# Performance work log

Measured on AMD Instinct MI355X. Metric: run time of the kernel, lower is better.

## Reference

```python
import jax, jax.numpy as jnp
import numpy as np

BETA = 5.5
MEM_FILLED = 25  # number of occupied slots per class; remaining slots are zero (empty)


def setup_inputs() -> dict:
    key = jax.random.key(0)
    ks = jax.random.split(key, 7)
    C, M, D = 1000, 50, 1024
    mem = jax.random.normal(ks[0], (C, M, D), jnp.float32)
    # emulate a partially-filled memory bank: slots >= MEM_FILLED are empty (all-zero rows)
    mem = mem * (jnp.arange(M)[None, :, None] < MEM_FILLED)
    return {
        "img_feat": jax.random.normal(ks[1], (1, D), jnp.float32),
        "image_feature_memory": mem,
        "fixed_global_feat_vanilla": jax.random.normal(ks[2], (C, 1, D), jnp.float32),
        "global_bias": 0.01 * jax.random.normal(ks[3], (C, D), jnp.float32),
        "global_bias_key": 0.01 * jax.random.normal(ks[4], (C, D), jnp.float32),
        "global_bias_value": 0.01 * jax.random.normal(ks[5], (C, D), jnp.float32),
        "global_ffn_bias": 0.01 * jax.random.normal(ks[6], (C, D), jnp.float32),
        "logit_scale": jnp.asarray(np.log(100.0), dtype=jnp.float32),
    }


def _l2norm(x, axis=-1):
    return x / jnp.linalg.norm(x, axis=axis, keepdims=True)


def reference(img_feat, image_feature_memory, fixed_global_feat_vanilla,
              global_bias, global_bias_key, global_bias_value,
              global_ffn_bias, logit_scale):
    # DualMem.get_image_pred, args.position == 'all', similarity_weighted classifier
    sg = jax.lax.stop_gradient  # torch.no_grad() block
    mem = jnp.concatenate([image_feature_memory, fixed_global_feat_vanilla], axis=1)  # (C, M+1, D)

    q = img_feat + jnp.mean(global_bias, axis=0, keepdims=True)      # (1, D)
    K = mem + global_bias_key[:, None, :]                             # (C, M+1, D)
    V = mem + global_bias_value[:, None, :]                           # (C, M+1, D)

    empty = (jnp.sum(mem, axis=-1) == 0)[..., None]                   # (C, M+1, 1) empty slots
    Kn = jnp.where(empty, 0.0, _l2norm(K))
    Vn = jnp.where(empty, 0.0, _l2norm(V))
    qn = _l2norm(q)
    qn, Kn, Vn = sg(qn), sg(Kn), sg(Vn)

    sim = jnp.exp(-BETA * (1.0 - jnp.einsum('d,cmd->cm', qn[0], Kn)))  # (C, M+1)
    adaptive = jnp.einsum('cm,cmd->cd', sim, Vn)                       # (C, D)
    adaptive = _l2norm(adaptive)
    adaptive = adaptive[None] + global_ffn_bias[None]                  # (1, C, D) position in {'output','all'}
    adaptive = _l2norm(adaptive)

    logits = jnp.exp(logit_scale) * jnp.einsum('bcd,bd->bc', adaptive, img_feat)  # (1, C)
    return jax.nn.softmax(logits, axis=1)
```

## Files before the change

### kernel.cpp

```cpp
#include <hip/hip_runtime.h>
#include <math.h>

#define BETA 5.5f
#define NC 1000
#define NM 51
#define ND 1024

typedef float nt_float4 __attribute__((ext_vector_type(4)));

__device__ __forceinline__ float wave_reduce_sum(float v) {
#pragma unroll
    for (int off = 32; off >= 1; off >>= 1) v += __shfl_xor(v, off, 64);
    return v;
}

__device__ __forceinline__ float block_reduce_sum(float v, float* red, int w, int lane) {
    v = wave_reduce_sum(v);
    __syncthreads();
    if (lane == 0) red[w] = v;
    __syncthreads();
    return red[0] + red[1] + red[2] + red[3];
}

__global__ __launch_bounds__(256) void colsum_part(const float* __restrict__ gb,
                                                   float* __restrict__ qpart) {
    const int t = threadIdx.x;
    const float4* p = (const float4*)(gb + (size_t)blockIdx.x * 25 * ND) + t;
    float4 s = make_float4(0.f, 0.f, 0.f, 0.f);
#pragma unroll
    for (int c = 0; c < 25; ++c) {
        float4 v = p[c * (ND / 4)];
        s.x += v.x; s.y += v.y; s.z += v.z; s.w += v.w;
    }
    ((float4*)qpart)[blockIdx.x * (ND / 4) + t] = s;
}

__global__ __launch_bounds__(256) void qnorm_kernel(const float* __restrict__ img,
                                                    const float* __restrict__ qpart,
                                                    float* __restrict__ qn) {
    __shared__ float red[8];
    const int t = threadIdx.x, w = t >> 6, lane = t & 63;
    float4 s = make_float4(0.f, 0.f, 0.f, 0.f);
#pragma unroll
    for (int p = 0; p < 40; ++p) {
        float4 v = ((const float4*)qpart)[p * (ND / 4) + t];
        s.x += v.x; s.y += v.y; s.z += v.z; s.w += v.w;
    }
    float4 iv = ((const float4*)img)[t];
    float4 q;
    q.x = iv.x + s.x * (1.f / NC);
    q.y = iv.y + s.y * (1.f / NC);
    q.z = iv.z + s.z * (1.f / NC);
    q.w = iv.w + s.w * (1.f / NC);
    float ssq = block_reduce_sum(q.x * q.x + q.y * q.y + q.z * q.z + q.w * q.w, red, w, lane);
    float r = rsqrtf(ssq);
    float4 o = make_float4(q.x * r, q.y * r, q.z * r, q.w * r);
    ((float4*)qn)[t] = o;
}

__global__ __launch_bounds__(256) void dualmem_main(
    const float* __restrict__ mem,
    const float* __restrict__ fixedg,
    const float* __restrict__ qn_g,
    const float* __restrict__ gbk,
    const float* __restrict__ gbv,
    float* __restrict__ accpart)
{
    __shared__ float lds_acc[4 * ND];

    const int c = blockIdx.x >> 1;
    const int half = blockIdx.x & 1;
    const int t = threadIdx.x;
    const int w = t >> 6;
    const int lane = t & 63;
    const int ww = half * 4 + w;

    float4 qn[4], bk[4], bv[4], acc[4];
    const float* bkp = gbk + (size_t)c * ND;
    const float* bvp = gbv + (size_t)c * ND;
#pragma unroll
    for (int j = 0; j < 4; ++j) {
        qn[j] = ((const float4*)qn_g)[j * 64 + lane];
        bk[j] = ((const float4*)bkp)[j * 64 + lane];
        bv[j] = ((const float4*)bvp)[j * 64 + lane];
        acc[j] = make_float4(0.f, 0.f, 0.f, 0.f);
    }

    nt_float4 cur[4], nxt[4];
    {
        const nt_float4* r = (ww < 50) ? (const nt_float4*)(mem + ((size_t)c * 50 + ww) * ND)
                                       : (const nt_float4*)(fixedg + (size_t)c * ND);
#pragma unroll
        for (int j = 0; j < 4; ++j) cur[j] = __builtin_nontemporal_load(&r[j * 64 + lane]);
    }

    for (int m = ww; m < NM; m += 8) {
        const int mn = m + 8;
        if (mn < NM) {
            const nt_float4* r = (mn < 50) ? (const nt_float4*)(mem + ((size_t)c * 50 + mn) * ND)
                                           : (const nt_float4*)(fixedg + (size_t)c * ND);
#pragma unroll
            for (int j = 0; j < 4; ++j) nxt[j] = __builtin_nontemporal_load(&r[j * 64 + lane]);
        }

        float sm = 0.f, ssqK = 0.f, dotK = 0.f, ssqV = 0.f;
#pragma unroll
        for (int j = 0; j < 4; ++j) {
            nt_float4 v = cur[j];
            sm += v.x + v.y + v.z + v.w;
            float kx = v.x + bk[j].x, ky = v.y + bk[j].y, kz = v.z + bk[j].z, kw = v.w + bk[j].w;
            ssqK += kx * kx + ky * ky + kz * kz + kw * kw;
            dotK += qn[j].x * kx + qn[j].y * ky + qn[j].z * kz + qn[j].w * kw;
            float vx = v.x + bv[j].x, vy = v.y + bv[j].y, vz = v.z + bv[j].z, vw = v.w + bv[j].w;
            ssqV += vx * vx + vy * vy + vz * vz + vw * vw;
        }
        sm   = wave_reduce_sum(sm);
        ssqK = wave_reduce_sum(ssqK);
        dotK = wave_reduce_sum(dotK);
        ssqV = wave_reduce_sum(ssqV);
        if (sm != 0.f) {
            float simv = expf(-BETA * (1.f - dotK * rsqrtf(ssqK)));
            float wt = simv * rsqrtf(ssqV);
#pragma unroll
            for (int j = 0; j < 4; ++j) {
                acc[j].x += wt * (cur[j].x + bv[j].x);
                acc[j].y += wt * (cur[j].y + bv[j].y);
                acc[j].z += wt * (cur[j].z + bv[j].z);
                acc[j].w += wt * (cur[j].w + bv[j].w);
            }
        }
#pragma unroll
        for (int j = 0; j < 4; ++j) cur[j] = nxt[j];
    }

#pragma unroll
    for (int j = 0; j < 4; ++j)
        ((float4*)lds_acc)[w * 256 + j * 64 + lane] = acc[j];
    __syncthreads();

    float4 a = make_float4(0.f, 0.f, 0.f, 0.f);
#pragma unroll
    for (int wv = 0; wv < 4; ++wv) {
        float4 p = ((float4*)lds_acc)[wv * 256 + t];
        a.x += p.x; a.y += p.y; a.z += p.z; a.w += p.w;
    }
    ((float4*)(accpart + (size_t)blockIdx.x * ND))[t] = a;
}

__global__ __launch_bounds__(256) void finalize_kernel(
    const float* __restrict__ img,
    const float* __restrict__ accpart,
    const float* __restrict__ ffn,
    const float* __restrict__ lsp,
    float* __restrict__ logits)
{
    __shared__ float red[8];
    const int c = blockIdx.x;
    const int t = threadIdx.x;
    const int w = t >> 6;
    const int lane = t & 63;

    float4 a0 = ((const float4*)(accpart + (size_t)(2 * c) * ND))[t];
    float4 a1 = ((const float4*)(accpart + (size_t)(2 * c + 1) * ND))[t];
    float4 a;
    a.x = a0.x + a1.x; a.y = a0.y + a1.y; a.z = a0.z + a1.z; a.w = a0.w + a1.w;

    float ssqA = block_reduce_sum(a.x * a.x + a.y * a.y + a.z * a.z + a.w * a.w, red, w, lane);
    float arn = rsqrtf(ssqA);
    float4 fv = ((const float4*)(ffn + (size_t)c * ND))[t];
    a.x = a.x * arn + fv.x;
    a.y = a.y * arn + fv.y;
    a.z = a.z * arn + fv.z;
    a.w = a.w * arn + fv.w;
    float ssqB = block_reduce_sum(a.x * a.x + a.y * a.y + a.z * a.z + a.w * a.w, red, w, lane);
    float brn = rsqrtf(ssqB);

    float4 iv = ((const float4*)img)[t];
    float dp = a.x * iv.x + a.y * iv.y + a.z * iv.z + a.w * iv.w;
    dp = block_reduce_sum(dp, red, w, lane);

    if (t == 0) logits[c] = expf(lsp[0]) * dp * brn;
}

__global__ __launch_bounds__(256) void softmax_kernel(const float* __restrict__ logits,
                                                      float* __restrict__ out) {
    __shared__ float red[8];
    int t = threadIdx.x, w = t >> 6, lane = t & 63;
    float l[4];
#pragma unroll
    for (int i = 0; i < 4; ++i) {
        int idx = t * 4 + i;
        l[i] = (idx < NC) ? logits[idx] : -3.402823466e+38f;
    }
    float mx = fmaxf(fmaxf(l[0], l[1]), fmaxf(l[2], l[3]));
#pragma unroll
    for (int off = 32; off >= 1; off >>= 1) mx = fmaxf(mx, __shfl_xor(mx, off, 64));
    __syncthreads();
    if (lane == 0) red[w] = mx;
    __syncthreads();
    mx = fmaxf(fmaxf(red[0], red[1]), fmaxf(red[2], red[3]));
    __syncthreads();

    float e[4], s = 0.f;
#pragma unroll
    for (int i = 0; i < 4; ++i) {
        int idx = t * 4 + i;
        e[i] = (idx < NC) ? expf(l[i] - mx) : 0.f;
        s += e[i];
    }
    s = block_reduce_sum(s, red, w, lane);
    float inv = 1.f / s;
#pragma unroll
    for (int i = 0; i < 4; ++i) {
        int idx = t * 4 + i;
        if (idx < NC) out[idx] = e[i] * inv;
    }
}

extern "C" void kernel_launch(void* const* d_in, const int* in_sizes, int n_in,
                              void* d_out, int out_size, void* d_ws, size_t ws_size,
                              hipStream_t stream) {
    const float* img    = (const float*)d_in[0];
    const float* mem    = (const float*)d_in[1];
    const float* fixedg = (const float*)d_in[2];
    const float* gb     = (const float*)d_in[3];
    const float* gbk    = (const float*)d_in[4];
    const float* gbv    = (const float*)d_in[5];
    const float* ffn    = (const float*)d_in[6];
    const float* ls     = (const float*)d_in[7];

    float* ws      = (float*)d_ws;
    float* qpart   = ws;
    float* qn      = ws + 40 * ND;
    float* accpart = ws + 41 * ND;
    float* logits  = accpart + 2000 * ND;
    float* out     = (float*)d_out;

    colsum_part<<<40, 256, 0, stream>>>(gb, qpart);
    qnorm_kernel<<<1, 256, 0, stream>>>(img, qpart, qn);
    dualmem_main<<<2 * NC, 256, 0, stream>>>(mem, fixedg, qn, gbk, gbv, accpart);
    finalize_kernel<<<NC, 256, 0, stream>>>(img, accpart, ffn, ls, logits);
    softmax_kernel<<<1, 256, 0, stream>>>(logits, out);
}
```

Baseline: 303.1 us.

## Fuse per-class memory attention with finalize into one 512-thread block

```diff
diff --git a/kernel.cpp b/kernel.cpp
--- a/kernel.cpp
+++ b/kernel.cpp
@@ -14,12 +14,20 @@
     return v;
 }
 
-__device__ __forceinline__ float block_reduce_sum(float v, float* red, int w, int lane) {
+__device__ __forceinline__ float block_reduce_sum4(float v, float* red, int w, int lane) {
     v = wave_reduce_sum(v);
     __syncthreads();
     if (lane == 0) red[w] = v;
     __syncthreads();
     return red[0] + red[1] + red[2] + red[3];
+}
+
+__device__ __forceinline__ float block_reduce_sum8(float v, float* red, int w, int lane) {
+    v = wave_reduce_sum(v);
+    __syncthreads();
+    if (lane == 0) red[w] = v;
+    __syncthreads();
+    return (red[0] + red[1] + red[2] + red[3]) + (red[4] + red[5] + red[6] + red[7]);
 }
 
 __global__ __launch_bounds__(256) void colsum_part(const float* __restrict__ gb,
@@ -52,28 +60,30 @@
     q.y = iv.y + s.y * (1.f / NC);
     q.z = iv.z + s.z * (1.f / NC);
     q.w = iv.w + s.w * (1.f / NC);
-    float ssq = block_reduce_sum(q.x * q.x + q.y * q.y + q.z * q.z + q.w * q.w, red, w, lane);
+    float ssq = block_reduce_sum4(q.x * q.x + q.y * q.y + q.z * q.z + q.w * q.w, red, w, lane);
     float r = rsqrtf(ssq);
     float4 o = make_float4(q.x * r, q.y * r, q.z * r, q.w * r);
     ((float4*)qn)[t] = o;
 }
 
-__global__ __launch_bounds__(256) void dualmem_main(
+__global__ __launch_bounds__(512) void dualmem_fused(
     const float* __restrict__ mem,
     const float* __restrict__ fixedg,
     const float* __restrict__ qn_g,
     const float* __restrict__ gbk,
     const float* __restrict__ gbv,
-    float* __restrict__ accpart)
+    const float* __restrict__ ffn,
+    const float* __restrict__ img,
+    const float* __restrict__ lsp,
+    float* __restrict__ logits)
 {
-    __shared__ float lds_acc[4 * ND];
-
-    const int c = blockIdx.x >> 1;
-    const int half = blockIdx.x & 1;
+    __shared__ float lds_acc[8 * ND];
+    __shared__ float red[8];
+
+    const int c = blockIdx.x;
     const int t = threadIdx.x;
     const int w = t >> 6;
     const int lane = t & 63;
-    const int ww = half * 4 + w;
 
     float4 qn[4], bk[4], bv[4], acc[4];
     const float* bkp = gbk + (size_t)c * ND;
@@ -88,13 +98,13 @@
 
     nt_float4 cur[4], nxt[4];
     {
-        const nt_float4* r = (ww < 50) ? (const nt_float4*)(mem + ((size_t)c * 50 + ww) * ND)
-                                       : (const nt_float4*)(fixedg + (size_t)c * ND);
+        const nt_float4* r = (w < 50) ? (const nt_float4*)(mem + ((size_t)c * 50 + w) * ND)
+                                      : (const nt_float4*)(fixedg + (size_t)c * ND);
 #pragma unroll
         for (int j = 0; j < 4; ++j) cur[j] = __builtin_nontemporal_load(&r[j * 64 + lane]);
     }
 
-    for (int m = ww; m < NM; m += 8) {
+    for (int m = w; m < NM; m += 8) {
         const int mn = m + 8;
         if (mn < NM) {
             const nt_float4* r = (mn < 50) ? (const nt_float4*)(mem + ((size_t)c * 50 + mn) * ND)
@@ -138,46 +148,29 @@
         ((float4*)lds_acc)[w * 256 + j * 64 + lane] = acc[j];
     __syncthreads();
 
-    float4 a = make_float4(0.f, 0.f, 0.f, 0.f);
+    float2 s0 = make_float2(0.f, 0.f), s1 = make_float2(0.f, 0.f);
 #pragma unroll
     for (int wv = 0; wv < 4; ++wv) {
-        float4 p = ((float4*)lds_acc)[wv * 256 + t];
-        a.x += p.x; a.y += p.y; a.z += p.z; a.w += p.w;
-    }
-    ((float4*)(accpart + (size_t)blockIdx.x * ND))[t] = a;
-}
-
-__global__ __launch_bounds__(256) void finalize_kernel(
-    const float* __restrict__ img,
-    const float* __restrict__ accpart,
-    const float* __restrict__ ffn,
-    const float* __restrict__ lsp,
-    float* __restrict__ logits)
-{
-    __shared__ float red[8];
-    const int c = blockIdx.x;
-    const int t = threadIdx.x;
-    const int w = t >> 6;
-    const int lane = t & 63;
-
-    float4 a0 = ((const float4*)(accpart + (size_t)(2 * c) * ND))[t];
-    float4 a1 = ((const float4*)(accpart + (size_t)(2 * c + 1) * ND))[t];
-    float4 a;
-    a.x = a0.x + a1.x; a.y = a0.y + a1.y; a.z = a0.z + a1.z; a.w = a0.w + a1.w;
-
-    float ssqA = block_reduce_sum(a.x * a.x + a.y * a.y + a.z * a.z + a.w * a.w, red, w, lane);
+        float2 p = ((const float2*)lds_acc)[wv * 512 + t];
+        s0.x += p.x; s0.y += p.y;
+    }
+#pragma unroll
+    for (int wv = 4; wv < 8; ++wv) {
+        float2 p = ((const float2*)lds_acc)[wv * 512 + t];
+        s1.x += p.x; s1.y += p.y;
+    }
+    float2 a = make_float2(s0.x + s1.x, s0.y + s1.y);
+
+    float ssqA = block_reduce_sum8(a.x * a.x + a.y * a.y, red, w, lane);
     float arn = rsqrtf(ssqA);
-    float4 fv = ((const float4*)(ffn + (size_t)c * ND))[t];
+    float2 fv = ((const float2*)(ffn + (size_t)c * ND))[t];
     a.x = a.x * arn + fv.x;
     a.y = a.y * arn + fv.y;
-    a.z = a.z * arn + fv.z;
-    a.w = a.w * arn + fv.w;
-    float ssqB = block_reduce_sum(a.x * a.x + a.y * a.y + a.z * a.z + a.w * a.w, red, w, lane);
+    float ssqB = block_reduce_sum8(a.x * a.x + a.y * a.y, red, w, lane);
     float brn = rsqrtf(ssqB);
 
-    float4 iv = ((const float4*)img)[t];
-    float dp = a.x * iv.x + a.y * iv.y + a.z * iv.z + a.w * iv.w;
-    dp = block_reduce_sum(dp, red, w, lane);
+    float2 iv = ((const float2*)img)[t];
+    float dp = block_reduce_sum8(a.x * iv.x + a.y * iv.y, red, w, lane);
 
     if (t == 0) logits[c] = expf(lsp[0]) * dp * brn;
 }
@@ -208,7 +201,7 @@
         e[i] = (idx < NC) ? expf(l[i] - mx) : 0.f;
         s += e[i];
     }
-    s = block_reduce_sum(s, red, w, lane);
+    s = block_reduce_sum4(s, red, w, lane);
     float inv = 1.f / s;
 #pragma unroll
     for (int i = 0; i < 4; ++i) {
@@ -232,13 +225,11 @@
     float* ws      = (float*)d_ws;
     float* qpart   = ws;
     float* qn      = ws + 40 * ND;
-    float* accpart = ws + 41 * ND;
-    float* logits  = accpart + 2000 * ND;
+    float* logits  = ws + 41 * ND;
     float* out     = (float*)d_out;
 
     colsum_part<<<40, 256, 0, stream>>>(gb, qpart);
     qnorm_kernel<<<1, 256, 0, stream>>>(img, qpart, qn);
-    dualmem_main<<<2 * NC, 256, 0, stream>>>(mem, fixedg, qn, gbk, gbv, accpart);
-    finalize_kernel<<<NC, 256, 0, stream>>>(img, accpart, ffn, ls, logits);
+    dualmem_fused<<<NC, 512, 0, stream>>>(mem, fixedg, qn, gbk, gbv, ffn, img, ls, logits);
     softmax_kernel<<<1, 256, 0, stream>>>(logits, out);
 }
```

After: 302.7 us. About the same (-0.1%).
